# Optimization experiments

Hardware: AMD Instinct MI355X
Metric: run time of the kernel (lower is better)

The kernel has to match this reference:

```python
import jax, jax.numpy as jnp
import numpy as np

RESET_PERIOD = 10
DECAY = 0.1
D_MODEL = 512
D_INNER = 1024
N_LAYERS = 4


def layer_norm(x, scale, bias, eps=1e-5):
    mu = jnp.mean(x, axis=-1, keepdims=True)
    var = jnp.mean((x - mu) ** 2, axis=-1, keepdims=True)
    return (x - mu) * jax.lax.rsqrt(var + eps) * scale + bias


def setup_inputs() -> dict:
    key = jax.random.key(0)
    ks = jax.random.split(key, 12)
    B, S, F, V, MF = 8, 2048, 128, 256, 4096
    D, DI, L = D_MODEL, D_INNER, N_LAYERS
    rn = lambda k, shape, s: jax.random.normal(k, shape, jnp.float32) * s
    return {
        "frames": rn(ks[0], (B, S, F), 1.0),
        "padding_mask": jax.random.uniform(ks[1], (B, S)) < 0.9,
        "W_in_proj": rn(ks[2], (F, D), 0.05),
        "b_in_proj": jnp.zeros((D,), jnp.float32),
        "pos_emb": rn(ks[3], (MF, D), 0.02),
        "ln_scale": jnp.ones((L, D), jnp.float32),
        "ln_bias": jnp.zeros((L, D), jnp.float32),
        "W_in": rn(ks[4], (L, D, 2 * DI), 0.03),
        "b_in": jnp.zeros((L, 2 * DI), jnp.float32),
        "W_out": rn(ks[5], (L, DI, D), 0.03),
        "b_out": jnp.zeros((L, D), jnp.float32),
        "fn_scale": jnp.ones((D,), jnp.float32),
        "fn_bias": jnp.zeros((D,), jnp.float32),
        "W_frame": rn(ks[6], (D, F), 0.03),
        "b_frame": jnp.zeros((F,), jnp.float32),
        "W_sym": rn(ks[7], (D, V), 0.03),
        "b_sym": jnp.zeros((V,), jnp.float32),
    }


def reference(frames, padding_mask, W_in_proj, b_in_proj, pos_emb,
              ln_scale, ln_bias, W_in, b_in, W_out, b_out,
              fn_scale, fn_bias, W_frame, b_frame, W_sym, b_sym):
    B, S, F = frames.shape
    # input projection + clamped positional embedding
    x = frames @ W_in_proj + b_in_proj                     # [B,S,D]
    pos = jnp.clip(jnp.arange(S), 0, pos_emb.shape[0] - 1)
    x = x + pos_emb[pos][None]
    # periodic hard-reset decay: frame_counter starts at 0, incremented AFTER
    # each step, so steps with (t+1) % reset_period == 0 are scaled.
    t = jnp.arange(S) + 1
    decay = jnp.where(t % RESET_PERIOD == 0, DECAY, 1.0)[None, :, None]  # [1,S,1]

    def layer(h, p):
        s, b, Wi, bi, Wo, bo = p
        n = layer_norm(h, s, b)
        uz = n @ Wi + bi                                   # [B,S,2*DI]
        u, g = jnp.split(uz, 2, axis=-1)
        y = (u * jax.nn.silu(g)) @ Wo + bo                 # [B,S,D]
        # wrapper scales the full block output (incl. residual)
        return (h + y) * decay, None

    x, _ = jax.lax.scan(layer, x, (ln_scale, ln_bias, W_in, b_in, W_out, b_out))
    x = layer_norm(x, fn_scale, fn_bias)
    frame_outputs = x @ W_frame + b_frame                  # [B,S,F]
    symbol_logits = x @ W_sym + b_sym                      # [B,S,V]
    m = padding_mask[..., None]
    frame_outputs = jnp.where(m, frame_outputs, 0.0)
    symbol_logits = jnp.where(m, symbol_logits, 0.0)
    return frame_outputs, symbol_logits
```

## Files before the change

kernel.cpp:

```cpp
#include <hip/hip_runtime.h>
#include <hip/hip_bf16.h>

using f32x4  = __attribute__((ext_vector_type(4))) float;
using bf16x8 = __attribute__((ext_vector_type(8))) short;
using bf16x4 = __attribute__((ext_vector_type(4))) short;

#define MTOT   16384
#define DMODEL 512
#define DINNER 1024
#define SEQ    2048

__device__ __forceinline__ short f2b(float f){
  unsigned u = __builtin_bit_cast(unsigned, f);
  u = (u + 0x7FFFu + ((u >> 16) & 1u)) >> 16;
  return (short)u;
}

__device__ __forceinline__ void gl_lds16(const short* g, short* l){
  __builtin_amdgcn_global_load_lds(
      (const __attribute__((address_space(1))) void*)g,
      (__attribute__((address_space(3))) void*)l, 16, 0, 0);
}

__global__ void detect_mask(const unsigned char* __restrict__ m, int* __restrict__ flag){
  __shared__ int sge2, soff, soff8;
  int tid = threadIdx.x;
  if (tid == 0){ sge2 = 0; soff = 0; soff8 = 0; }
  __syncthreads();
  int ge2 = 0, off = 0, off8 = 0;
  for (int i = tid; i < 16384; i += 256){
    unsigned char b = m[i];
    if (b >= 2) ge2++;
    if ((i & 3) && b) off++;
    if (((i & 7) == 4) && b) off8++;
  }
  atomicAdd(&sge2, ge2); atomicAdd(&soff, off); atomicAdd(&soff8, off8);
  __syncthreads();
  if (tid == 0){
    int f;
    if      (sge2 > 0) f = 2;
    else if (soff > 0) f = 1;
    else if (soff8 > 0) f = 0;
    else               f = 3;
    *flag = f;
  }
}

__device__ __forceinline__ bool mask_at(const void* mask, int flag, int m){
  if (flag == 1) return ((const unsigned char*)mask)[m] != 0;
  if (flag == 2) return ((const float*)mask)[m] != 0.0f;
  if (flag == 3) return ((const int*)mask)[2*m] != 0;
  return ((const int*)mask)[m] != 0;
}

__global__ void cvt_bf16(const float* __restrict__ in, short* __restrict__ out){
  int i = (blockIdx.x * 256 + threadIdx.x) * 4;
  float4 v = *(const float4*)(in + i);
  bf16x4 o; o[0] = f2b(v.x); o[1] = f2b(v.y); o[2] = f2b(v.z); o[3] = f2b(v.w);
  *(bf16x4*)(out + i) = o;
}

template<int GLU>
__global__ void transpose_w(const float* __restrict__ in, short* __restrict__ out, int R, int C){
  in  += (size_t)blockIdx.z * R * C;
  out += (size_t)blockIdx.z * R * C;
  __shared__ float t[32][33];
  int tx = threadIdx.x, ty = threadIdx.y;
  int r0 = blockIdx.y * 32, c0 = blockIdx.x * 32;
  #pragma unroll
  for (int i = 0; i < 4; i++)
    t[ty + i*8][tx] = in[(size_t)(r0 + ty + i*8) * C + c0 + tx];
  __syncthreads();
  #pragma unroll
  for (int i = 0; i < 4; i++){
    int oc = c0 + ty + i*8;
    int nr;
    if constexpr (GLU){
      int half = C >> 1;
      nr = (oc < half) ? (((oc >> 4) << 5) + (oc & 15))
                       : ((((oc - half) >> 4) << 5) + 16 + (oc & 15));
    } else nr = oc;
    out[(size_t)nr * R + r0 + tx] = f2b(t[tx][ty + i*8]);
  }
}

__global__ __launch_bounds__(256) void ln_k(const float* __restrict__ x,
                                            const float* __restrict__ sc,
                                            const float* __restrict__ bi,
                                            short* __restrict__ out){
  int row  = blockIdx.x * 4 + (threadIdx.x >> 6);
  int lane = threadIdx.x & 63;
  const float* p = x + (size_t)row * DMODEL + lane * 8;
  float4 a = *(const float4*)p;
  float4 b = *(const float4*)(p + 4);
  float s = a.x+a.y+a.z+a.w + b.x+b.y+b.z+b.w;
  float q = a.x*a.x+a.y*a.y+a.z*a.z+a.w*a.w + b.x*b.x+b.y*b.y+b.z*b.z+b.w*b.w;
  #pragma unroll
  for (int o = 32; o >= 1; o >>= 1){ s += __shfl_xor(s, o); q += __shfl_xor(q, o); }
  float mu  = s * (1.0f/DMODEL);
  float var = q * (1.0f/DMODEL) - mu*mu;
  float rs  = rsqrtf(var + 1e-5f);
  int c = lane * 8;
  float vals[8] = {a.x,a.y,a.z,a.w,b.x,b.y,b.z,b.w};
  bf16x8 o8;
  #pragma unroll
  for (int e = 0; e < 8; e++) o8[e] = f2b((vals[e]-mu)*rs*sc[c+e] + bi[c+e]);
  *(bf16x8*)(out + (size_t)row * DMODEL + c) = o8;
}

template<int K>
__global__ __launch_bounds__(512, 2) void glu8p(
    const short* __restrict__ A, const short* __restrict__ B,
    const float* __restrict__ bias, short* __restrict__ obuf)
{
  constexpr int NT = K / 64;
  constexpr int HT = NT * 4;
  __shared__ short lds[8 * 8192];

  const int nbx = gridDim.x;
  int bid = blockIdx.y * nbx + blockIdx.x;
  const int nwg = nbx * gridDim.y;
  bid = (bid & 7) * (nwg >> 3) + (bid >> 3);
  const int n0 = (bid % nbx) * 256, m0 = (bid / nbx) * 256;

  const int tid = threadIdx.x, lane = tid & 63, wid = tid >> 6;
  const int wr = wid >> 2, wc = wid & 3;
  const int fr = lane & 15, kg = lane >> 4;

  f32x4 acc[8][2][2];
  const f32x4 zero = {0.f, 0.f, 0.f, 0.f};
  #pragma unroll
  for (int i = 0; i < 8; i++)
    #pragma unroll
    for (int nh = 0; nh < 2; nh++)
      #pragma unroll
      for (int j = 0; j < 2; j++) acc[i][nh][j] = zero;

  const int rl0 = wid * 8 + (lane >> 3);
  const int swz = ((lane & 7) ^ ((lane >> 3) & 7)) * 8;
  const short* Ab = A + ((size_t)m0 + rl0) * K + swz;
  const short* Bb = B + ((size_t)n0 + rl0) * K + swz;

  auto stage = [&](int h){
    if (h < HT){
      const int q = h & 3, kt = h >> 2, slot = h & 7;
      const short* src = (q < 2) ? (Ab + (size_t)(q * 128) * K + kt * 64)
                                 : (Bb + (size_t)((q - 2) * 128) * K + kt * 64);
      short* dst = lds + slot * 8192 + wid * 512;
      gl_lds16(src, dst);
      gl_lds16(src + (size_t)64 * K, dst + 4096);
    }
  };

  #pragma unroll
  for (int h = 0; h < 6; h++) stage(h);
  asm volatile("s_waitcnt vmcnt(4)" ::: "memory");
  __builtin_amdgcn_sched_barrier(0);
  __builtin_amdgcn_s_barrier();
  __builtin_amdgcn_sched_barrier(0);

  for (int kt = 0; kt < NT; ++kt){
    bf16x8 aF[8];
    #pragma unroll
    for (int p = 0; p < 4; ++p){
      const int kb = p >> 1, nh = p & 1;
      const int ks = kg + kb * 4;
      if (nh == 0){
        const int slot = (4 * kt + wr) & 7;
        #pragma unroll
        for (int i = 0; i < 8; i++)
          aF[i] = *(const bf16x8*)((const char*)lds + slot * 16384
                     + (i * 16 + fr) * 128 + ((ks ^ (fr & 7)) * 16));
      }
      bf16x8 bF[2];
      {
        const int slot = (4 * kt + 2 + nh) & 7;
        #pragma unroll
        for (int j = 0; j < 2; j++)
          bF[j] = *(const bf16x8*)((const char*)lds + slot * 16384
                     + (wc * 32 + j * 16 + fr) * 128 + ((ks ^ (fr & 7)) * 16));
      }
      stage(4 * kt + p + 6);
      if (p == 3){
        if (kt < NT - 2)       asm volatile("s_waitcnt vmcnt(4)" ::: "memory");
        else if (kt == NT - 2) asm volatile("s_waitcnt vmcnt(0)" ::: "memory");
      }
      __builtin_amdgcn_sched_barrier(0);
      __builtin_amdgcn_s_barrier();
      __builtin_amdgcn_sched_barrier(0);
      __builtin_amdgcn_s_setprio(1);
      #pragma unroll
      for (int i = 0; i < 8; i++)
        #pragma unroll
        for (int j = 0; j < 2; j++)
          acc[i][nh][j] = __builtin_amdgcn_mfma_f32_16x16x32_bf16(aF[i], bF[j], acc[i][nh][j], 0, 0, 0);
      __builtin_amdgcn_s_setprio(0);
      __builtin_amdgcn_sched_barrier(0);
      __builtin_amdgcn_s_barrier();
      __builtin_amdgcn_sched_barrier(0);
    }
  }

  #pragma unroll
  for (int i = 0; i < 8; i++){
    #pragma unroll
    for (int nh = 0; nh < 2; nh++){
      const int pc = n0 + nh * 128 + wc * 32;
      const int lc = ((pc >> 5) << 4) + fr;
      #pragma unroll
      for (int r = 0; r < 4; r++){
        const int gm = m0 + wr * 128 + i * 16 + kg * 4 + r;
        float u = acc[i][nh][0][r] + bias[lc];
        float g = acc[i][nh][1][r] + bias[1024 + lc];
        float sg = g / (1.0f + expf(-g));
        obuf[(size_t)gm * 1024 + lc] = f2b(u * sg);
      }
    }
  }
}

template<int MODE, int K>
__global__ __launch_bounds__(256) void gemm_k(
    const short* __restrict__ A, const short* __restrict__ B,
    const float* __restrict__ bias0, const float* __restrict__ bias1,
    const float* __restrict__ pos, float* __restrict__ xbuf, short* __restrict__ obuf,
    float* __restrict__ fout, const void* __restrict__ mask, const int* __restrict__ flagp,
    int ldo)
{
  constexpr int BM = 128, BN = 128;
  __shared__ short lds[(BM + BN) * 64];
  short* lA = lds;
  short* lB = lds + BM * 64;

  const int nbx = gridDim.x;
  int bid = blockIdx.y * nbx + blockIdx.x;
  const int nwg = nbx * gridDim.y;
  bid = (bid & 7) * (nwg >> 3) + (bid >> 3);
  const int bx = bid % nbx, by = bid / nbx;
  const int n0 = bx * BN, m0 = by * BM;

  const int tid = threadIdx.x, lane = tid & 63, wid = tid >> 6;
  const int lr  = lane >> 3;
  const int lks = (lane & 7) ^ (lr & 7);
  const int fr = lane & 15;
  const int kg = lane >> 4;

  const int wr = wid >> 1, wc = wid & 1;
  const int rA0 = wr * 64 + fr;
  const int rB0 = wc * 64 + fr;

  f32x4 acc[4][4];
  const f32x4 zero = {0.f, 0.f, 0.f, 0.f};
  #pragma unroll
  for (int i = 0; i < 4; i++)
    #pragma unroll
    for (int j = 0; j < 4; j++) acc[i][j] = zero;

  const short* Ab = A + (size_t)m0 * K + (size_t)lr * K + lks * 8;
  const short* Bb = B + (size_t)n0 * K + (size_t)lr * K + lks * 8;

  for (int kt = 0; kt < K; kt += 64){
    __syncthreads();
    #pragma unroll
    for (int c = 0; c < 4; c++)
      gl_lds16(Ab + kt + (size_t)(wid + c * 4) * 8 * K, lA + (wid + c * 4) * 512);
    #pragma unroll
    for (int c = 0; c < 4; c++)
      gl_lds16(Bb + kt + (size_t)(wid + c * 4) * 8 * K, lB + (wid + c * 4) * 512);
    __syncthreads();

    #pragma unroll
    for (int kb8 = 0; kb8 < 8; kb8 += 4){
      bf16x8 aF[4], bF[4];
      #pragma unroll
      for (int i = 0; i < 4; i++){
        const int row = rA0 + i * 16;
        aF[i] = *(const bf16x8*)((const char*)lA + row * 128 + (((kg + kb8) ^ (row & 7)) * 16));
      }
      #pragma unroll
      for (int j = 0; j < 4; j++){
        const int row = rB0 + j * 16;
        bF[j] = *(const bf16x8*)((const char*)lB + row * 128 + (((kg + kb8) ^ (row & 7)) * 16));
      }
      #pragma unroll
      for (int i = 0; i < 4; i++)
        #pragma unroll
        for (int j = 0; j < 4; j++)
          acc[i][j] = __builtin_amdgcn_mfma_f32_16x16x32_bf16(aF[i], bF[j], acc[i][j], 0, 0, 0);
    }
  }

  const int col0 = n0 + wc * 64 + fr;
  const int row0 = m0 + wr * 64 + kg * 4;
  int flag = 0;
  if constexpr (MODE == 3) flag = *flagp;

  #pragma unroll
  for (int i = 0; i < 4; i++){
    #pragma unroll
    for (int r = 0; r < 4; r++){
      const int gm = row0 + i * 16 + r;
      #pragma unroll
      for (int j = 0; j < 4; j++){
        const int gn = col0 + j * 16;
        float v = acc[i][j][r];
        if constexpr (MODE == 0){
          xbuf[(size_t)gm * ldo + gn] = v + bias0[gn] + pos[(size_t)(gm & (SEQ-1)) * DMODEL + gn];
        } else if constexpr (MODE == 2){
          int s = gm & (SEQ-1);
          float d = (((s + 1) % 10) == 0) ? 0.1f : 1.0f;
          float y = v + bias0[gn];
          xbuf[(size_t)gm * ldo + gn] = (xbuf[(size_t)gm * ldo + gn] + y) * d;
        } else {
          bool mk = mask_at(mask, flag, gm);
          if (gn < 128){
            fout[(size_t)gm * 128 + gn] = mk ? (v + bias0[gn]) : 0.0f;
          } else {
            int gs = gn - 128;
            fout[(size_t)16384 * 128 + (size_t)gm * 256 + gs] = mk ? (v + bias1[gs]) : 0.0f;
          }
        }
      }
    }
  }
}

extern "C" void kernel_launch(void* const* d_in, const int* in_sizes, int n_in,
                              void* d_out, int out_size, void* d_ws, size_t ws_size,
                              hipStream_t stream){
  const float* frames    = (const float*)d_in[0];
  const void*  mask      = d_in[1];
  const float* W_in_proj = (const float*)d_in[2];
  const float* b_in_proj = (const float*)d_in[3];
  const float* pos_emb   = (const float*)d_in[4];
  const float* ln_scale  = (const float*)d_in[5];
  const float* ln_bias   = (const float*)d_in[6];
  const float* W_in      = (const float*)d_in[7];
  const float* b_in      = (const float*)d_in[8];
  const float* W_out     = (const float*)d_in[9];
  const float* b_out     = (const float*)d_in[10];
  const float* fn_scale  = (const float*)d_in[11];
  const float* fn_bias   = (const float*)d_in[12];
  const float* W_frame   = (const float*)d_in[13];
  const float* b_frame   = (const float*)d_in[14];
  const float* W_sym     = (const float*)d_in[15];
  const float* b_sym     = (const float*)d_in[16];

  char* w = (char*)d_ws;
  int*   flag = (int*)w;
  float* xbuf = (float*)(w + 256);
  short* nbuf = (short*)(w + 256 + 33554432);
  short* abuf = (short*)(w + 256 + 33554432 + 16777216);
  short* frb  = (short*)(w + 256 + 33554432 + 16777216 + 33554432);
  short* Wt0  = frb + (size_t)16384 * 128;
  short* Wt1  = Wt0 + (size_t)512 * 128;
  short* Wt2  = Wt1 + (size_t)4 * 2048 * 512;
  short* Wt3  = Wt2 + (size_t)4 * 512 * 1024;
  short* Wt4  = Wt3 + (size_t)128 * 512;

  detect_mask<<<1, 256, 0, stream>>>((const unsigned char*)mask, flag);
  cvt_bf16<<<2048, 256, 0, stream>>>(frames, frb);
  transpose_w<0><<<dim3(16,  4, 1), dim3(32, 8), 0, stream>>>(W_in_proj, Wt0, 128, 512);
  transpose_w<1><<<dim3(64, 16, 4), dim3(32, 8), 0, stream>>>(W_in,      Wt1, 512, 2048);
  transpose_w<0><<<dim3(16, 32, 4), dim3(32, 8), 0, stream>>>(W_out,     Wt2, 1024, 512);
  transpose_w<0><<<dim3(4,  16, 1), dim3(32, 8), 0, stream>>>(W_frame,   Wt3, 512, 128);
  transpose_w<0><<<dim3(8,  16, 1), dim3(32, 8), 0, stream>>>(W_sym,     Wt4, 512, 256);

  gemm_k<0, 128><<<dim3(4, 128), 256, 0, stream>>>(frb, Wt0, b_in_proj, nullptr, pos_emb,
      xbuf, nullptr, nullptr, nullptr, nullptr, 512);

  for (int l = 0; l < 4; l++){
    ln_k<<<4096, 256, 0, stream>>>(xbuf, ln_scale + l*512, ln_bias + l*512, nbuf);
    glu8p<512><<<dim3(8, 64), 512, 0, stream>>>(nbuf,
        Wt1 + (size_t)l*2048*512, b_in + l*2048, abuf);
    gemm_k<2, 1024><<<dim3(4, 128), 256, 0, stream>>>(abuf, Wt2 + (size_t)l*512*1024,
        b_out + l*512, nullptr, nullptr, xbuf, nullptr, nullptr, nullptr, nullptr, 512);
  }

  ln_k<<<4096, 256, 0, stream>>>(xbuf, fn_scale, fn_bias, nbuf);
  gemm_k<3, 512><<<dim3(3, 128), 256, 0, stream>>>(nbuf, Wt3, b_frame, b_sym, nullptr,
      nullptr, nullptr, (float*)d_out, mask, flag, 0);
}
```

Measured before the change: 526.9 us.

## Add multi-stage pipelined 8-wave kernel for residual output GEMM

Replaces the generic 128x128 gemm_k used for the per-layer output projection with a new 512-thread kernel that computes 128x256 tiles. It uses a 9-slot LDS ring with direct global-to-LDS loads issued two K-tiles ahead, XOR-swizzled rows, and a grid remap for block locality. The residual add, bias and periodic decay are fused into its epilogue. It also drops sched_barrier fences around the barriers in the existing GLU kernel, which lets the compiler reorder code across them at some risk to the intended load/MFMA interleave. The grid shrinks to 256 blocks, so there are fewer workgroups to spread across the CUs.

```diff
diff --git a/kernel.cpp b/kernel.cpp
--- a/kernel.cpp
+++ b/kernel.cpp
@@ -155,9 +155,7 @@
   #pragma unroll
   for (int h = 0; h < 6; h++) stage(h);
   asm volatile("s_waitcnt vmcnt(4)" ::: "memory");
-  __builtin_amdgcn_sched_barrier(0);
   __builtin_amdgcn_s_barrier();
-  __builtin_amdgcn_sched_barrier(0);
 
   for (int kt = 0; kt < NT; ++kt){
     bf16x8 aF[8];
@@ -185,9 +183,7 @@
         if (kt < NT - 2)       asm volatile("s_waitcnt vmcnt(4)" ::: "memory");
         else if (kt == NT - 2) asm volatile("s_waitcnt vmcnt(0)" ::: "memory");
       }
-      __builtin_amdgcn_sched_barrier(0);
       __builtin_amdgcn_s_barrier();
-      __builtin_amdgcn_sched_barrier(0);
       __builtin_amdgcn_s_setprio(1);
       #pragma unroll
       for (int i = 0; i < 8; i++)
@@ -195,9 +191,7 @@
         for (int j = 0; j < 2; j++)
           acc[i][nh][j] = __builtin_amdgcn_mfma_f32_16x16x32_bf16(aF[i], bF[j], acc[i][nh][j], 0, 0, 0);
       __builtin_amdgcn_s_setprio(0);
-      __builtin_amdgcn_sched_barrier(0);
       __builtin_amdgcn_s_barrier();
-      __builtin_amdgcn_sched_barrier(0);
     }
   }
 
@@ -214,6 +208,114 @@
         float g = acc[i][nh][1][r] + bias[1024 + lc];
         float sg = g / (1.0f + expf(-g));
         obuf[(size_t)gm * 1024 + lc] = f2b(u * sg);
+      }
+    }
+  }
+}
+
+template<int K>
+__global__ __launch_bounds__(512, 2) void res8p(
+    const short* __restrict__ A, const short* __restrict__ B,
+    const float* __restrict__ bias, float* __restrict__ xbuf)
+{
+  constexpr int NT = K / 64;
+  __shared__ short lds[9 * 8192];
+
+  const int nbx = gridDim.x;
+  int bid = blockIdx.y * nbx + blockIdx.x;
+  const int nwg = nbx * gridDim.y;
+  bid = (bid & 7) * (nwg >> 3) + (bid >> 3);
+  const int n0 = (bid % nbx) * 256, m0 = (bid / nbx) * 128;
+
+  const int lane = threadIdx.x & 63, wid = threadIdx.x >> 6;
+  const int wr = wid >> 2, wc = wid & 3;
+  const int fr = lane & 15, kg = lane >> 4;
+
+  f32x4 acc[4][4];
+  const f32x4 zero = {0.f, 0.f, 0.f, 0.f};
+  #pragma unroll
+  for (int i = 0; i < 4; i++)
+    #pragma unroll
+    for (int j = 0; j < 4; j++) acc[i][j] = zero;
+
+  const int rl0 = wid * 8 + (lane >> 3);
+  const int swz = ((lane & 7) ^ ((lane >> 3) & 7)) * 8;
+  const short* Ab = A + ((size_t)m0 + rl0) * K + swz;
+  const short* Bb = B + ((size_t)n0 + rl0) * K + swz;
+
+  auto stage_tile = [&](int m){
+    if (m < NT){
+      const int s0 = (3 * m) % 9;
+      short* d0 = lds + s0 * 8192 + wid * 512;
+      const short* gA = Ab + m * 64;
+      gl_lds16(gA, d0);
+      gl_lds16(gA + (size_t)64 * K, d0 + 4096);
+      const int s1 = (3 * m + 1) % 9;
+      short* d1 = lds + s1 * 8192 + wid * 512;
+      const short* gB0 = Bb + m * 64;
+      gl_lds16(gB0, d1);
+      gl_lds16(gB0 + (size_t)64 * K, d1 + 4096);
+      const int s2 = (3 * m + 2) % 9;
+      short* d2 = lds + s2 * 8192 + wid * 512;
+      const short* gB1 = Bb + (size_t)128 * K + m * 64;
+      gl_lds16(gB1, d2);
+      gl_lds16(gB1 + (size_t)64 * K, d2 + 4096);
+    }
+  };
+
+  stage_tile(0); stage_tile(1);
+  asm volatile("s_waitcnt vmcnt(6)" ::: "memory");
+  __builtin_amdgcn_s_barrier();
+
+  for (int kt = 0; kt < NT; ++kt){
+    const int sA = (3 * kt) % 9;
+    const int sB = (3 * kt + 1 + (wc >> 1)) % 9;
+    #pragma unroll
+    for (int kb = 0; kb < 2; kb++){
+      const int ks = kg + kb * 4;
+      bf16x8 aF[4], bF[4];
+      #pragma unroll
+      for (int i = 0; i < 4; i++){
+        const int row = wr * 64 + i * 16 + fr;
+        aF[i] = *(const bf16x8*)((const char*)lds + sA * 16384
+                   + row * 128 + ((ks ^ (row & 7)) * 16));
+      }
+      #pragma unroll
+      for (int j = 0; j < 4; j++){
+        const int row = (wc & 1) * 64 + j * 16 + fr;
+        bF[j] = *(const bf16x8*)((const char*)lds + sB * 16384
+                   + row * 128 + ((ks ^ (row & 7)) * 16));
+      }
+      if (kb == 0){
+        stage_tile(kt + 2);
+      } else {
+        if (kt < NT - 2)       asm volatile("s_waitcnt vmcnt(6)" ::: "memory");
+        else if (kt == NT - 2) asm volatile("s_waitcnt vmcnt(0)" ::: "memory");
+      }
+      __builtin_amdgcn_s_barrier();
+      __builtin_amdgcn_s_setprio(1);
+      #pragma unroll
+      for (int i = 0; i < 4; i++)
+        #pragma unroll
+        for (int j = 0; j < 4; j++)
+          acc[i][j] = __builtin_amdgcn_mfma_f32_16x16x32_bf16(aF[i], bF[j], acc[i][j], 0, 0, 0);
+      __builtin_amdgcn_s_setprio(0);
+      __builtin_amdgcn_s_barrier();
+    }
+  }
+
+  #pragma unroll
+  for (int i = 0; i < 4; i++){
+    #pragma unroll
+    for (int r = 0; r < 4; r++){
+      const int gm = m0 + wr * 64 + i * 16 + kg * 4 + r;
+      const int s = gm & (SEQ - 1);
+      const float d = (((s + 1) % 10) == 0) ? 0.1f : 1.0f;
+      #pragma unroll
+      for (int j = 0; j < 4; j++){
+        const int gn = n0 + wc * 64 + j * 16 + fr;
+        const float y = acc[i][j][r] + bias[gn];
+        xbuf[(size_t)gm * 512 + gn] = (xbuf[(size_t)gm * 512 + gn] + y) * d;
       }
     }
   }
@@ -306,11 +408,6 @@
         float v = acc[i][j][r];
         if constexpr (MODE == 0){
           xbuf[(size_t)gm * ldo + gn] = v + bias0[gn] + pos[(size_t)(gm & (SEQ-1)) * DMODEL + gn];
-        } else if constexpr (MODE == 2){
-          int s = gm & (SEQ-1);
-          float d = (((s + 1) % 10) == 0) ? 0.1f : 1.0f;
-          float y = v + bias0[gn];
-          xbuf[(size_t)gm * ldo + gn] = (xbuf[(size_t)gm * ldo + gn] + y) * d;
         } else {
           bool mk = mask_at(mask, flag, gm);
           if (gn < 128){
@@ -373,8 +470,8 @@
     ln_k<<<4096, 256, 0, stream>>>(xbuf, ln_scale + l*512, ln_bias + l*512, nbuf);
     glu8p<512><<<dim3(8, 64), 512, 0, stream>>>(nbuf,
         Wt1 + (size_t)l*2048*512, b_in + l*2048, abuf);
-    gemm_k<2, 1024><<<dim3(4, 128), 256, 0, stream>>>(abuf, Wt2 + (size_t)l*512*1024,
-        b_out + l*512, nullptr, nullptr, xbuf, nullptr, nullptr, nullptr, nullptr, 512);
+    res8p<1024><<<dim3(2, 128), 512, 0, stream>>>(abuf, Wt2 + (size_t)l*512*1024,
+        b_out + l*512, xbuf);
   }
 
   ln_k<<<4096, 256, 0, stream>>>(xbuf, fn_scale, fn_bias, nbuf);
```

After: 519.3 us. No clear change (-1.4%).
